# Optimization experiments

Measured on AMD Instinct MI355X. Metric: run time of the kernel, lower is better.

## Reference

```python
import jax, jax.numpy as jnp
import numpy as np

EPS_PROX = 5.0   # proximal epsilon from __init__
BN_EPS = 1e-5    # torch BatchNorm1d default eps
STRIDE = 3


def setup_inputs() -> dict:
    key = jax.random.key(0)
    ks = jax.random.split(key, 9)
    B, T, D = 64, 768, 128     # batch, timesteps, input_size
    E, H, O, K = 64, 128, 10, 3  # embedding_dim, hidden, output, kernel
    Tc = (T - K) // STRIDE + 1   # 256 conv output steps
    s_ih = 1.0 / np.sqrt(H)
    return {
        "inputs": jax.random.normal(ks[0], (B, T, D), jnp.float32),
        "r": jax.random.normal(ks[1], (B, E, Tc), jnp.float32),
        "conv_w": jax.random.normal(ks[2], (E, D, K), jnp.float32) * (1.0 / np.sqrt(D * K)),
        "conv_b": jnp.zeros((E,), jnp.float32),
        "bn_gamma": jnp.ones((E,), jnp.float32),
        "bn_beta": jnp.zeros((E,), jnp.float32),
        "w_ih": jax.random.normal(ks[3], (4 * H, E), jnp.float32) * s_ih,
        "w_hh": jax.random.normal(ks[4], (4 * H, H), jnp.float32) * s_ih,
        "b_ih": jax.random.normal(ks[5], (4 * H,), jnp.float32) * s_ih,
        "b_hh": jax.random.normal(ks[6], (4 * H,), jnp.float32) * s_ih,
        "lin_w": jax.random.normal(ks[7], (O, H), jnp.float32) * s_ih,
        "lin_b": jnp.zeros((O,), jnp.float32),
        "batch_size": B,
    }


def _forward(inputs, conv_w, conv_b, bn_gamma, bn_beta,
             w_ih, w_hh, b_ih, b_hh, lin_w, lin_b):
    # F.normalize(inputs, dim=2): L2 normalize feature dim
    nrm = jnp.sqrt(jnp.sum(inputs * inputs, axis=2, keepdims=True))
    x = inputs / jnp.maximum(nrm, 1e-12)
    x = jnp.transpose(x, (0, 2, 1))  # [B, D, T]
    # Conv1d(D -> E, kernel=3, stride=3)
    emb = jax.lax.conv_general_dilated(
        x, conv_w, window_strides=(STRIDE,), padding='VALID',
        dimension_numbers=('NCH', 'OIH', 'NCH')) + conv_b[None, :, None]
    # BatchNorm1d in training mode: batch stats over (B, T')
    mean = jnp.mean(emb, axis=(0, 2), keepdims=True)
    var = jnp.var(emb, axis=(0, 2), keepdims=True)
    emb = (emb - mean) * jax.lax.rsqrt(var + BN_EPS)
    emb = emb * bn_gamma[None, :, None] + bn_beta[None, :, None]
    act = jax.nn.relu(emb)               # [B, E, T']
    xs = jnp.transpose(act, (2, 0, 1))   # [T', B, E] scan over time

    H = w_hh.shape[1]
    Wi, Wf, Wg, Wo = jnp.split(w_ih, 4, axis=0)  # torch gate order i,f,g,o
    I_H = jnp.eye(H, dtype=inputs.dtype)

    def step(carry, x_t):
        h, c = carry
        z = x_t @ w_ih.T + b_ih + h @ w_hh.T + b_hh  # [B, 4H]
        zi, zf, zg, zo = jnp.split(z, 4, axis=1)
        i = jax.nn.sigmoid(zi)
        f = jax.nn.sigmoid(zf)
        g = jnp.tanh(zg)
        o = jax.nn.sigmoid(zo)
        s = f * c + i * g                            # pre-prox cell state
        # Analytic Jacobian G = ds/dx_t : [B, H, E]
        G = ((i * (1 - i) * g)[:, :, None] * Wi[None]
             + (f * (1 - f) * c)[:, :, None] * Wf[None]
             + (i * (1 - g * g))[:, :, None] * Wg[None])
        # Proximal update: c = (I + eps * G G^T)^{-1} s
        A = I_H + EPS_PROX * jnp.einsum('bhe,bke->bhk', G, G)
        c_new = jnp.linalg.solve(A, s[:, :, None])[:, :, 0]
        h_new = o * jnp.tanh(c_new)
        return (h_new, c_new), None

    B = xs.shape[1]
    init = (jnp.zeros((B, H), inputs.dtype), jnp.zeros((B, H), inputs.dtype))
    (h_last, _), _ = jax.lax.scan(step, init, xs)
    return h_last @ lin_w.T + lin_b  # [B, output_size]


def reference(inputs, r, conv_w, conv_b, bn_gamma, bn_beta,
              w_ih, w_hh, b_ih, b_hh, lin_w, lin_b, batch_size):
    # mode='ProxLSTM'; r and batch_size are unused in this branch (r is only
    # added to the embedding in 'plain' mode).
    return _forward(inputs, conv_w, conv_b, bn_gamma, bn_beta,
                    w_ih, w_hh, b_ih, b_hh, lin_w, lin_b)
```

## Files before the change

### kernel.cpp

```cpp
#include <hip/hip_runtime.h>
#include <math.h>

#define EPSP 5.0f
#define BNEPS 1e-5f
constexpr int B_  = 64;
constexpr int T_  = 768;
constexpr int D_  = 128;
constexpr int E_  = 64;
constexpr int H_  = 128;
constexpr int FH_ = 512;
constexpr int TC_ = 256;
constexpr int O_  = 10;

constexpr size_t EMB_OFF   = 0;
constexpr size_t SUM_OFF   = EMB_OFF + (size_t)B_ * TC_ * E_;
constexpr size_t SCL_OFF   = SUM_OFF + 128;
constexpr size_t CWT_OFF   = SCL_OFF + 128;
constexpr size_t WHIF_OFF  = CWT_OFF + (size_t)E_ * D_ * 3;
constexpr size_t WLO8F_OFF = WHIF_OFF + 32768;
constexpr size_t WTHI_OFF  = WLO8F_OFF + 16384;
constexpr size_t WTLO8_OFF = WTHI_OFF + 12288;
constexpr size_t ZX_OFF    = WTLO8_OFF + 6144;
constexpr size_t WS_FLOATS = ZX_OFF + (size_t)B_ * TC_ * FH_;

typedef __bf16 bf16x8 __attribute__((ext_vector_type(8)));
typedef float  floatx4 __attribute__((ext_vector_type(4)));

__device__ inline float fast_rcp(float x) { return __builtin_amdgcn_rcpf(x); }
__device__ inline float frsq(float x) { return __builtin_amdgcn_rsqf(x); }
__device__ inline float fexp2(float x) { return __builtin_amdgcn_exp2f(x); }
__device__ inline float rl(float v, int lane) {
  return __int_as_float(__builtin_amdgcn_readlane(__float_as_int(v), lane));
}
#define LOG2E 1.4426950408889634f
__device__ inline float fsigmoid(float x) { return fast_rcp(1.f + fexp2(-LOG2E * x)); }
__device__ inline float ftanh(float x) { return 1.f - 2.f * fast_rcp(1.f + fexp2(2.f * LOG2E * x)); }

__device__ inline unsigned char enc8(float v) {
  unsigned b = __float_as_uint(v);
  unsigned s = b >> 31;
  int e = (int)((b >> 23) & 0xFF) - 127;
  if (e < -6) return 0;
  unsigned m3 = (b >> 20) & 7;
  return (unsigned char)((s << 7) | ((unsigned)(e + 7) << 3) | m3);
}
#define S18 3.814697265625e-06f

__global__ void prep_kernel(const float* __restrict__ conv_w,
                            const float* __restrict__ w_hh,
                            float* __restrict__ ws) {
  int gid = blockIdx.x * blockDim.x + threadIdx.x;
  int nthr = gridDim.x * blockDim.x;
  for (int i = gid; i < 128; i += nthr) ws[SUM_OFF + i] = 0.f;
  __bf16* whiF = (__bf16*)(ws + WHIF_OFF);
  unsigned char* wlo8F = (unsigned char*)(ws + WLO8F_OFF);
  for (int s = gid; s < 512 * 128; s += nthr) {
    int st = s >> 7, r2 = s & 127, f = r2 >> 3, j = r2 & 7;
    int wv = st >> 6, lane = st & 63, m = lane & 15, q = lane >> 4;
    int rti = f >> 2, kt = f & 3;
    int R = wv * 64 + rti * 16 + m;
    int k = kt * 32 + q * 8 + j;
    float w = w_hh[(size_t)R * 128 + k];
    __bf16 hi = (__bf16)w;
    whiF[s] = hi;
    wlo8F[s] = enc8((w - (float)hi) * 16384.f);
  }
  for (int s = gid; s < E_ * D_ * 3; s += nthr) {
    int e = s / 384; int r = s - e * 384; int d = r / 3; int k = r - d * 3;
    ws[CWT_OFF + ((size_t)k * D_ + d) * E_ + e] = conv_w[s];
  }
}

__global__ __launch_bounds__(256) void conv_bn_kernel(const float* __restrict__ inputs,
                                                      const float* __restrict__ conv_b,
                                                      float* __restrict__ ws) {
  __shared__ float xin[48 * 129];
  __shared__ float rnorm[48];
  __shared__ float cwc[3 * 16 * 64];
  __shared__ float bnr1[256], bnr2[256];
  int tid = threadIdx.x;
  int bb = blockIdx.x >> 4, tcg = blockIdx.x & 15;
  const float* inp = inputs + ((size_t)bb * T_ + (size_t)tcg * 48) * D_;
  for (int idx = tid; idx < 48 * 128; idx += 256) {
    int r = idx >> 7, d = idx & 127;
    xin[r * 129 + d] = inp[idx];
  }
  __syncthreads();
  if (tid < 48) {
    float ss = 0.f;
    for (int d = 0; d < 128; ++d) { float v = xin[tid * 129 + d]; ss += v * v; }
    rnorm[tid] = 1.0f / fmaxf(sqrtf(ss), 1e-12f);
  }
  __syncthreads();
  for (int idx = tid; idx < 48 * 128; idx += 256) {
    int r = idx >> 7, d = idx & 127;
    xin[r * 129 + d] *= rnorm[r];
  }
  int e = tid & 63, tg = tid >> 6;
  float cb = conv_b[e];
  float acc[4];
#pragma unroll
  for (int q = 0; q < 4; ++q) acc[q] = cb;
  for (int ch = 0; ch < 8; ++ch) {
    __syncthreads();
    for (int idx = tid; idx < 3072; idx += 256) {
      int k = idx >> 10; int i2 = idx & 1023; int dd = i2 >> 6; int e2 = i2 & 63;
      cwc[idx] = ws[CWT_OFF + ((size_t)k * D_ + ch * 16 + dd) * E_ + e2];
    }
    __syncthreads();
    for (int dd = 0; dd < 16; ++dd) {
      int dcol = ch * 16 + dd;
#pragma unroll
      for (int k = 0; k < 3; ++k) {
        float w = cwc[(k * 16 + dd) * 64 + e];
#pragma unroll
        for (int q = 0; q < 4; ++q) {
          int tcl = tg * 4 + q;
          acc[q] += w * xin[(3 * tcl + k) * 129 + dcol];
        }
      }
    }
  }
  float ps = 0.f, pss = 0.f;
#pragma unroll
  for (int q = 0; q < 4; ++q) {
    int tcl = tg * 4 + q;
    ws[EMB_OFF + ((size_t)bb * TC_ + tcg * 16 + tcl) * E_ + e] = acc[q];
    ps += acc[q]; pss += acc[q] * acc[q];
  }
  bnr1[tg * 64 + e] = ps;
  bnr2[tg * 64 + e] = pss;
  __syncthreads();
  if (tid < 64) {
    float s1 = bnr1[tid] + bnr1[64 + tid] + bnr1[128 + tid] + bnr1[192 + tid];
    float s2 = bnr2[tid] + bnr2[64 + tid] + bnr2[128 + tid] + bnr2[192 + tid];
    atomicAdd(&ws[SUM_OFF + tid], s1);
    atomicAdd(&ws[SUM_OFF + 64 + tid], s2);
  }
}

__global__ void bn_finalize_kernel(const float* __restrict__ gamma,
                                   const float* __restrict__ beta,
                                   float* __restrict__ ws) {
  int e = threadIdx.x;
  if (e < 64) {
    const float n = (float)(B_ * TC_);
    float mean = ws[SUM_OFF + e] / n;
    float var = ws[SUM_OFF + 64 + e] / n - mean * mean;
    float sc = gamma[e] * rsqrtf(var + BNEPS);
    ws[SCL_OFF + e] = sc;
    ws[SCL_OFF + 64 + e] = beta[e] - mean * sc;
  }
}

__global__ __launch_bounds__(256) void zx_kernel(const float* __restrict__ w_ih,
                                                 const float* __restrict__ b_ih,
                                                 const float* __restrict__ b_hh,
                                                 float* __restrict__ ws) {
  __shared__ __align__(16) float actT[16 * 64];
  int tid = threadIdx.x;
  int bb = blockIdx.x >> 4, tg2 = blockIdx.x & 15;
  for (int idx = tid; idx < 1024; idx += 256) {
    int tl = idx >> 6, e2 = idx & 63;
    float v = ws[EMB_OFF + ((size_t)bb * TC_ + tg2 * 16 + tl) * E_ + e2];
    actT[idx] = fmaxf(v * ws[SCL_OFF + e2] + ws[SCL_OFF + 64 + e2], 0.f);
  }
  __syncthreads();
  int j0 = tid, j1 = tid + 256;
  float acc0[16], acc1[16];
  float bias0 = b_ih[j0] + b_hh[j0];
  float bias1 = b_ih[j1] + b_hh[j1];
#pragma unroll
  for (int tl = 0; tl < 16; ++tl) { acc0[tl] = bias0; acc1[tl] = bias1; }
  for (int e4 = 0; e4 < 16; ++e4) {
    float4 w0 = *(const float4*)(w_ih + (size_t)j0 * 64 + e4 * 4);
    float4 w1 = *(const float4*)(w_ih + (size_t)j1 * 64 + e4 * 4);
#pragma unroll
    for (int tl = 0; tl < 16; ++tl) {
      float4 a4 = *(const float4*)(actT + tl * 64 + e4 * 4);
      acc0[tl] += w0.x * a4.x + w0.y * a4.y + w0.z * a4.z + w0.w * a4.w;
      acc1[tl] += w1.x * a4.x + w1.y * a4.y + w1.z * a4.z + w1.w * a4.w;
    }
  }
#pragma unroll
  for (int tl = 0; tl < 16; ++tl) {
    size_t base = ZX_OFF + ((size_t)bb * TC_ + tg2 * 16 + tl) * FH_;
    ws[base + j0] = acc0[tl];
    ws[base + j1] = acc1[tl];
  }
}

template <int NCT>
__device__ inline void gram_do(int rt, int ct0, int lane,
                               const __bf16* GtHi, const __bf16* GtLo,
                               float* M_s, float* y_s) {
  int m = lane & 15, q = lane >> 4;
  bf16x8 AH[4], AL[4];
#pragma unroll
  for (int kt = 0; kt < 4; ++kt) {
    AH[kt] = *(const bf16x8*)(GtHi + (rt * 16 + m) * 136 + kt * 32 + q * 8);
    AL[kt] = *(const bf16x8*)(GtLo + (rt * 16 + m) * 136 + kt * 32 + q * 8);
  }
  floatx4 C[NCT];
#pragma unroll
  for (int ci = 0; ci < NCT; ++ci) C[ci] = (floatx4){0.f, 0.f, 0.f, 0.f};
#pragma unroll
  for (int ci = 0; ci < NCT; ++ci) {
#pragma unroll
    for (int kt = 0; kt < 4; ++kt) {
      bf16x8 BH = *(const bf16x8*)(GtHi + ((ct0 + ci) * 16 + m) * 136 + kt * 32 + q * 8);
      bf16x8 BL = *(const bf16x8*)(GtLo + ((ct0 + ci) * 16 + m) * 136 + kt * 32 + q * 8);
      C[ci] = __builtin_amdgcn_mfma_f32_16x16x32_bf16(AH[kt], BH, C[ci], 0, 0, 0);
      C[ci] = __builtin_amdgcn_mfma_f32_16x16x32_bf16(AH[kt], BL, C[ci], 0, 0, 0);
      C[ci] = __builtin_amdgcn_mfma_f32_16x16x32_bf16(AL[kt], BH, C[ci], 0, 0, 0);
    }
  }
#pragma unroll
  for (int ci = 0; ci < NCT; ++ci) {
    int ct = ct0 + ci;
#pragma unroll
    for (int reg = 0; reg < 4; ++reg) {
      int grow = rt * 16 + q * 4 + reg;
      if (ct < 4) {
        int gcol = ct * 16 + m;
        M_s[grow * 65 + gcol] = EPSP * C[ci][reg] + ((grow == gcol) ? 1.f : 0.f);
      } else if (m == 0) {
        y_s[grow] = C[ci][reg];
      }
    }
  }
}

#define LD8(dst, base) { float4 _a = *(const float4*)(base); float4 _b = *(const float4*)((base) + 4); \
  dst[0]=_a.x; dst[1]=_a.y; dst[2]=_a.z; dst[3]=_a.w; dst[4]=_b.x; dst[5]=_b.y; dst[6]=_b.z; dst[7]=_b.w; }

union U4L { uint4 u; long l[2]; };

__global__ __launch_bounds__(512, 2)
void scan_kernel(const float* __restrict__ w_ih,
                 const float* __restrict__ lin_w,
                 const float* __restrict__ lin_b,
                 const float* __restrict__ ws,
                 float* __restrict__ out) {
  __shared__ __align__(16) __bf16 GtHi[80 * 136], GtLo[80 * 136];
  __shared__ __align__(16) __bf16 hbH[128], hbL[128];
  __shared__ __align__(8)  unsigned char hb8[128];
  __shared__ float M_s[64 * 65];
  __shared__ float Lp2_s[2 * 16 * 64];
  __shared__ __align__(16) float z0_s[512], zx_s[512];
  __shared__ __align__(16) float s_s[128], o_s[128], c_s[128], h_s[128];
  __shared__ float y_s[64];
  __shared__ __align__(8) float x_s[64];
  __shared__ __align__(16) unsigned char W8L[512 * 128];

  const int tid = threadIdx.x;
  const int bb = blockIdx.x;
  const int lane = tid & 63;
  const int wv = tid >> 6;
  const int m = lane & 15, q = lane >> 4;
  const int hg = tid >> 5;
  const int ep = tid & 31;
  const int h0 = hg * 8, e0 = ep * 2;

  float Wr[3][2][8];
#pragma unroll
  for (int g = 0; g < 3; ++g)
#pragma unroll
    for (int e = 0; e < 2; ++e) {
      const float* bse = w_ih + ((size_t)(g * 128 + h0)) * 64 + e0 + e;
#pragma unroll
      for (int r = 0; r < 8; ++r) Wr[g][e][r] = bse[(size_t)r * 64];
    }

  bf16x8 WH[4][4];
  {
    const uint4* whip = (const uint4*)(ws + WHIF_OFF) + (size_t)tid * 16;
#pragma unroll
    for (int rti = 0; rti < 4; ++rti)
#pragma unroll
      for (int kt = 0; kt < 4; ++kt) {
        uint4 t4 = whip[rti * 4 + kt];
        WH[rti][kt] = __builtin_bit_cast(bf16x8, t4);
      }
  }
  {
    const uint4* src = (const uint4*)(ws + WLO8F_OFF) + (size_t)tid * 8;
    uint4* dst = (uint4*)W8L;
#pragma unroll
    for (int f = 0; f < 8; ++f) dst[f * 512 + tid] = src[f];
  }
  for (int i = tid; i < 15 * 136; i += 512) { GtHi[65 * 136 + i] = (__bf16)0.f; GtLo[65 * 136 + i] = (__bf16)0.f; }
  if (tid < 128) {
    c_s[tid] = 0.f; h_s[tid] = 0.f;
    hbH[tid] = (__bf16)0.f; hbL[tid] = (__bf16)0.f; hb8[tid] = 0;
  }
  const float* zxp = ws + ZX_OFF + (size_t)bb * TC_ * FH_;
  float dinv = 1.f;
  bf16x8 ZB;
#pragma unroll
  for (int j = 0; j < 8; ++j) ZB[j] = (__bf16)0.f;
  float zxcur = zxp[tid];
  __syncthreads();

  for (int t = 0; t < TC_; ++t) {
    {
      zx_s[tid] = zxcur;
      if (t + 1 < TC_) zxcur = zxp[(size_t)(t + 1) * FH_ + tid];
      long B8[4];
#pragma unroll
      for (int kt = 0; kt < 4; ++kt)
        B8[kt] = (m == 0) ? *(const long*)(hb8 + kt * 32 + q * 8) : 0L;
      floatx4 C[4];
#pragma unroll
      for (int h2 = 0; h2 < 2; ++h2) {
        U4L wa[4];
#pragma unroll
        for (int i = 0; i < 4; ++i) wa[i].u = ((const uint4*)W8L)[(h2 * 4 + i) * 512 + tid];
        floatx4 C8a = {0,0,0,0}, C8b = {0,0,0,0};
#pragma unroll
        for (int kt = 0; kt < 4; ++kt) {
          long A0 = wa[(0 * 4 + kt) >> 1].l[kt & 1];
          long A1 = wa[(1 * 4 + kt) >> 1].l[kt & 1];
          C8a = __builtin_amdgcn_mfma_f32_16x16x32_fp8_fp8(A0, B8[kt], C8a, 0, 0, 0);
          C8b = __builtin_amdgcn_mfma_f32_16x16x32_fp8_fp8(A1, B8[kt], C8b, 0, 0, 0);
        }
        C[h2 * 2 + 0] = C8a * S18;
        C[h2 * 2 + 1] = C8b * S18;
      }
#pragma unroll
      for (int p = 0; p < 2; ++p) {
        const __bf16* hb = p ? hbL : hbH;
#pragma unroll
        for (int kt = 0; kt < 4; ++kt) {
          bf16x8 Bf = (m == 0) ? *(const bf16x8*)(hb + kt * 32 + q * 8) : ZB;
#pragma unroll
          for (int rti = 0; rti < 4; ++rti)
            C[rti] = __builtin_amdgcn_mfma_f32_16x16x32_bf16(WH[rti][kt], Bf, C[rti], 0, 0, 0);
        }
      }
      if (m == 0) {
#pragma unroll
        for (int rti = 0; rti < 4; ++rti)
          *(floatx4*)(z0_s + wv * 64 + rti * 16 + q * 4) = C[rti];
      }
    }
    __syncthreads();
    float gva[2][8];
    {
      float zA[8], xA[8], zi[8], zf[8], zg[8], zo[8], cc[8];
      LD8(zA, z0_s + h0) LD8(xA, zx_s + h0)
#pragma unroll
      for (int r = 0; r < 8; ++r) zi[r] = zA[r] + xA[r];
      LD8(zA, z0_s + 128 + h0) LD8(xA, zx_s + 128 + h0)
#pragma unroll
      for (int r = 0; r < 8; ++r) zf[r] = zA[r] + xA[r];
      LD8(zA, z0_s + 256 + h0) LD8(xA, zx_s + 256 + h0)
#pragma unroll
      for (int r = 0; r < 8; ++r) zg[r] = zA[r] + xA[r];
      LD8(zA, z0_s + 384 + h0) LD8(xA, zx_s + 384 + h0)
#pragma unroll
      for (int r = 0; r < 8; ++r) zo[r] = zA[r] + xA[r];
      LD8(cc, c_s + h0)
      float a1[8], a2[8], a3[8], sv[8], ov[8];
#pragma unroll
      for (int r = 0; r < 8; ++r) {
        float ig = fsigmoid(zi[r]);
        float fg = fsigmoid(zf[r]);
        float gg = ftanh(zg[r]);
        sv[r] = fg * cc[r] + ig * gg;
        ov[r] = fsigmoid(zo[r]);
        a1[r] = ig * (1.f - ig) * gg;
        a2[r] = fg * (1.f - fg) * cc[r];
        a3[r] = ig * (1.f - gg * gg);
      }
      if (ep == 0) {
        *(float4*)(s_s + h0)     = (float4){sv[0], sv[1], sv[2], sv[3]};
        *(float4*)(s_s + h0 + 4) = (float4){sv[4], sv[5], sv[6], sv[7]};
        *(float4*)(o_s + h0)     = (float4){ov[0], ov[1], ov[2], ov[3]};
        *(float4*)(o_s + h0 + 4) = (float4){ov[4], ov[5], ov[6], ov[7]};
        bf16x8 sh, sl;
#pragma unroll
        for (int r = 0; r < 8; ++r) {
          __bf16 hi = (__bf16)sv[r];
          sh[r] = hi; sl[r] = (__bf16)(sv[r] - (float)hi);
        }
        *(bf16x8*)(GtHi + 64 * 136 + h0) = sh;
        *(bf16x8*)(GtLo + 64 * 136 + h0) = sl;
      }
#pragma unroll
      for (int e = 0; e < 2; ++e) {
        int col = e0 + e;
        bf16x8 gh, gl;
#pragma unroll
        for (int r = 0; r < 8; ++r) {
          float gv = a1[r] * Wr[0][e][r] + a2[r] * Wr[1][e][r] + a3[r] * Wr[2][e][r];
          gva[e][r] = gv;
          __bf16 hi = (__bf16)gv;
          gh[r] = hi; gl[r] = (__bf16)(gv - (float)hi);
        }
        *(bf16x8*)(GtHi + col * 136 + h0) = gh;
        *(bf16x8*)(GtLo + col * 136 + h0) = gl;
      }
    }
    __syncthreads();
    if (wv < 4) gram_do<3>(wv, 0, lane, GtHi, GtLo, M_s, y_s);
    else        gram_do<2>(wv - 4, 3, lane, GtHi, GtLo, M_s, y_s);
    __syncthreads();
#pragma unroll 1
    for (int pan = 0; pan < 4; ++pan) {
      int j0 = pan * 16;
      float* Lpw = Lp2_s + (pan & 1) * (16 * 64);
      float* Lpr = Lp2_s + (((pan & 1) ^ 1)) * (16 * 64);
      if (tid < 64) {
        float p[16];
#pragma unroll
        for (int jj = 0; jj < 16; ++jj) p[jj] = M_s[lane * 65 + j0 + jj];
#pragma unroll
        for (int jj = 0; jj < 16; ++jj) {
          float d  = rl(p[jj], j0 + jj);
          float rs = frsq(d);
          p[jj] *= rs;
          dinv = (lane == j0 + jj) ? rs : dinv;
          M_s[lane * 65 + j0 + jj] = (lane > j0 + jj) ? p[jj] * rs : 0.f;
          Lpw[jj * 64 + lane] = p[jj];
#pragma unroll
          for (int kk = jj + 1; kk < 16; ++kk) {
            float l = rl(p[jj], j0 + kk);
            p[kk] -= p[jj] * l;
          }
        }
        if (pan == 3) {
          float r = y_s[lane];
#pragma unroll 16
          for (int i = 0; i < 64; ++i) {
            float Ai = M_s[lane * 65 + i];
            r -= Ai * rl(r, i);
          }
          float tau = r * dinv * dinv;
#pragma unroll 16
          for (int i = 63; i >= 0; --i) {
            float Bi = M_s[i * 65 + lane];
            tau -= Bi * rl(tau, i);
          }
          x_s[lane] = tau;
        }
      } else if (pan >= 1) {
        int k0 = 16 * pan + 16;
        if (k0 < 64) {
          float Lrow[16];
#pragma unroll
          for (int jj = 0; jj < 16; ++jj) Lrow[jj] = Lpr[jj * 64 + lane];
          for (int k = k0 + (wv - 1); k < 64; k += 7) {
            float acc = M_s[lane * 65 + k];
#pragma unroll
            for (int jj = 0; jj < 16; ++jj) acc -= Lrow[jj] * Lpr[jj * 64 + k];
            M_s[lane * 65 + k] = acc;
          }
        }
      }
      __syncthreads();
      if (pan < 3) {
        float Lrow[16];
#pragma unroll
        for (int jj = 0; jj < 16; ++jj) Lrow[jj] = Lpw[jj * 64 + lane];
#pragma unroll
        for (int kk2 = 0; kk2 < 2; ++kk2) {
          int k = j0 + 16 + wv * 2 + kk2;
          float acc = M_s[lane * 65 + k];
#pragma unroll
          for (int jj = 0; jj < 16; ++jj) acc -= Lrow[jj] * Lpw[jj * 64 + k];
          M_s[lane * 65 + k] = acc;
        }
        __syncthreads();
      }
    }
    {
      float2 xl = *(const float2*)(x_s + e0);
      float u0[8];
#pragma unroll
      for (int r = 0; r < 8; ++r) u0[r] = gva[0][r] * xl.x + gva[1][r] * xl.y;
#pragma unroll
      for (int sft = 1; sft < 32; sft <<= 1)
#pragma unroll
        for (int r = 0; r < 8; ++r) u0[r] += __shfl_xor(u0[r], sft, 32);
      if (ep == 0) {
        float cn[8], hn[8];
        bf16x8 hh8, hl8;
        unsigned long long h8v = 0ULL;
#pragma unroll
        for (int r = 0; r < 8; ++r) {
          cn[r] = s_s[h0 + r] - EPSP * u0[r];
          hn[r] = o_s[h0 + r] * ftanh(cn[r]);
          __bf16 hi = (__bf16)hn[r];
          hh8[r] = hi; hl8[r] = (__bf16)(hn[r] - (float)hi);
          h8v |= ((unsigned long long)enc8(hn[r] * 16.f)) << (8 * r);
        }
        *(float4*)(c_s + h0)     = (float4){cn[0], cn[1], cn[2], cn[3]};
        *(float4*)(c_s + h0 + 4) = (float4){cn[4], cn[5], cn[6], cn[7]};
        *(float4*)(h_s + h0)     = (float4){hn[0], hn[1], hn[2], hn[3]};
        *(float4*)(h_s + h0 + 4) = (float4){hn[4], hn[5], hn[6], hn[7]};
        *(bf16x8*)(hbH + h0) = hh8;
        *(bf16x8*)(hbL + h0) = hl8;
        *(unsigned long long*)(hb8 + h0) = h8v;
      }
    }
    __syncthreads();
  }
  if (tid < O_) {
    float acc = lin_b[tid];
    for (int hh2 = 0; hh2 < 128; ++hh2) acc += h_s[hh2] * lin_w[tid * 128 + hh2];
    out[(size_t)bb * O_ + tid] = acc;
  }
}

extern "C" void kernel_launch(void* const* d_in, const int* in_sizes, int n_in,
                              void* d_out, int out_size, void* d_ws, size_t ws_size,
                              hipStream_t stream) {
  (void)in_sizes; (void)n_in; (void)out_size;
  const float* inputs  = (const float*)d_in[0];
  const float* conv_w  = (const float*)d_in[2];
  const float* conv_b  = (const float*)d_in[3];
  const float* gamma   = (const float*)d_in[4];
  const float* beta    = (const float*)d_in[5];
  const float* w_ih    = (const float*)d_in[6];
  const float* w_hh    = (const float*)d_in[7];
  const float* b_ih    = (const float*)d_in[8];
  const float* b_hh    = (const float*)d_in[9];
  const float* lin_w   = (const float*)d_in[10];
  const float* lin_b   = (const float*)d_in[11];
  float* out = (float*)d_out;
  float* ws  = (float*)d_ws;

  if (ws_size < WS_FLOATS * sizeof(float)) return;

  hipLaunchKernelGGL(prep_kernel, dim3(192), dim3(256), 0, stream, conv_w, w_hh, ws);
  hipLaunchKernelGGL(conv_bn_kernel, dim3(1024), dim3(256), 0, stream, inputs, conv_b, ws);
  hipLaunchKernelGGL(bn_finalize_kernel, dim3(1), dim3(64), 0, stream, gamma, beta, ws);
  hipLaunchKernelGGL(zx_kernel, dim3(1024), dim3(256), 0, stream, w_ih, b_ih, b_hh, ws);
  hipLaunchKernelGGL(scan_kernel, dim3(64), dim3(512), 0, stream, w_ih, lin_w, lin_b, ws, out);
}
```

Baseline: 4.632 ms.

## Switch Cholesky to LDL^T form and fuse BN finalize into zx kernel

The in-loop Cholesky factorization of the per-step 64x64 Gram system is rewritten as an LDL^T-style factorization that uses a reciprocal of the pivot instead of a reciprocal square root. Pivot reciprocals are stored in a small shared buffer and folded into the trailing-update rows. This shortens the serial dependency chain on the single factorizing wave. Separately, the BatchNorm finalize kernel is removed and its per-channel scale and shift are recomputed in each zx block, which saves one kernel launch at the cost of some redundant work per block.

New measurement: 4.897 ms. 1.06x slower.

```diff
diff --git a/kernel.cpp b/kernel.cpp
--- a/kernel.cpp
+++ b/kernel.cpp
@@ -139,31 +139,29 @@
   }
 }
 
-__global__ void bn_finalize_kernel(const float* __restrict__ gamma,
-                                   const float* __restrict__ beta,
-                                   float* __restrict__ ws) {
-  int e = threadIdx.x;
-  if (e < 64) {
-    const float n = (float)(B_ * TC_);
-    float mean = ws[SUM_OFF + e] / n;
-    float var = ws[SUM_OFF + 64 + e] / n - mean * mean;
-    float sc = gamma[e] * rsqrtf(var + BNEPS);
-    ws[SCL_OFF + e] = sc;
-    ws[SCL_OFF + 64 + e] = beta[e] - mean * sc;
-  }
-}
-
 __global__ __launch_bounds__(256) void zx_kernel(const float* __restrict__ w_ih,
                                                  const float* __restrict__ b_ih,
                                                  const float* __restrict__ b_hh,
+                                                 const float* __restrict__ gamma,
+                                                 const float* __restrict__ beta,
                                                  float* __restrict__ ws) {
   __shared__ __align__(16) float actT[16 * 64];
+  __shared__ float scl[128];
   int tid = threadIdx.x;
   int bb = blockIdx.x >> 4, tg2 = blockIdx.x & 15;
+  if (tid < 64) {
+    const float n = (float)(B_ * TC_);
+    float mean = ws[SUM_OFF + tid] / n;
+    float var = ws[SUM_OFF + 64 + tid] / n - mean * mean;
+    float sc = gamma[tid] * rsqrtf(var + BNEPS);
+    scl[tid] = sc;
+    scl[64 + tid] = beta[tid] - mean * sc;
+  }
+  __syncthreads();
   for (int idx = tid; idx < 1024; idx += 256) {
     int tl = idx >> 6, e2 = idx & 63;
     float v = ws[EMB_OFF + ((size_t)bb * TC_ + tg2 * 16 + tl) * E_ + e2];
-    actT[idx] = fmaxf(v * ws[SCL_OFF + e2] + ws[SCL_OFF + 64 + e2], 0.f);
+    actT[idx] = fmaxf(v * scl[e2] + scl[64 + e2], 0.f);
   }
   __syncthreads();
   int j0 = tid, j1 = tid + 256;
@@ -247,6 +245,7 @@
   __shared__ __align__(8)  unsigned char hb8[128];
   __shared__ float M_s[64 * 65];
   __shared__ float Lp2_s[2 * 16 * 64];
+  __shared__ float dp2_s[2 * 16];
   __shared__ __align__(16) float z0_s[512], zx_s[512];
   __shared__ __align__(16) float s_s[128], o_s[128], c_s[128], h_s[128];
   __shared__ float y_s[64];
@@ -411,6 +410,8 @@
       int j0 = pan * 16;
       float* Lpw = Lp2_s + (pan & 1) * (16 * 64);
       float* Lpr = Lp2_s + (((pan & 1) ^ 1)) * (16 * 64);
+      float* dpw = dp2_s + (pan & 1) * 16;
+      float* dpr = dp2_s + (((pan & 1) ^ 1)) * 16;
       if (tid < 64) {
         float p[16];
 #pragma unroll
@@ -418,15 +419,15 @@
 #pragma unroll
         for (int jj = 0; jj < 16; ++jj) {
           float d  = rl(p[jj], j0 + jj);
-          float rs = frsq(d);
-          p[jj] *= rs;
-          dinv = (lane == j0 + jj) ? rs : dinv;
-          M_s[lane * 65 + j0 + jj] = (lane > j0 + jj) ? p[jj] * rs : 0.f;
+          float di = fast_rcp(d);
+          dinv = (lane == j0 + jj) ? di : dinv;
+          M_s[lane * 65 + j0 + jj] = (lane > j0 + jj) ? p[jj] * di : 0.f;
           Lpw[jj * 64 + lane] = p[jj];
+          if (lane == j0 + jj) dpw[jj] = di;
 #pragma unroll
           for (int kk = jj + 1; kk < 16; ++kk) {
-            float l = rl(p[jj], j0 + kk);
-            p[kk] -= p[jj] * l;
+            float s = rl(p[jj], j0 + kk) * di;
+            p[kk] -= p[jj] * s;
           }
         }
         if (pan == 3) {
@@ -436,7 +437,7 @@
             float Ai = M_s[lane * 65 + i];
             r -= Ai * rl(r, i);
           }
-          float tau = r * dinv * dinv;
+          float tau = r * dinv;
 #pragma unroll 16
           for (int i = 63; i >= 0; --i) {
             float Bi = M_s[i * 65 + lane];
@@ -449,7 +450,7 @@
         if (k0 < 64) {
           float Lrow[16];
 #pragma unroll
-          for (int jj = 0; jj < 16; ++jj) Lrow[jj] = Lpr[jj * 64 + lane];
+          for (int jj = 0; jj < 16; ++jj) Lrow[jj] = Lpr[jj * 64 + lane] * dpr[jj];
           for (int k = k0 + (wv - 1); k < 64; k += 7) {
             float acc = M_s[lane * 65 + k];
 #pragma unroll
@@ -462,7 +463,7 @@
       if (pan < 3) {
         float Lrow[16];
 #pragma unroll
-        for (int jj = 0; jj < 16; ++jj) Lrow[jj] = Lpw[jj * 64 + lane];
+        for (int jj = 0; jj < 16; ++jj) Lrow[jj] = Lpw[jj * 64 + lane] * dpw[jj];
 #pragma unroll
         for (int kk2 = 0; kk2 < 2; ++kk2) {
           int k = j0 + 16 + wv * 2 + kk2;
@@ -535,7 +536,6 @@
 
   hipLaunchKernelGGL(prep_kernel, dim3(192), dim3(256), 0, stream, conv_w, w_hh, ws);
   hipLaunchKernelGGL(conv_bn_kernel, dim3(1024), dim3(256), 0, stream, inputs, conv_b, ws);
-  hipLaunchKernelGGL(bn_finalize_kernel, dim3(1), dim3(64), 0, stream, gamma, beta, ws);
-  hipLaunchKernelGGL(zx_kernel, dim3(1024), dim3(256), 0, stream, w_ih, b_ih, b_hh, ws);
+  hipLaunchKernelGGL(zx_kernel, dim3(1024), dim3(256), 0, stream, w_ih, b_ih, b_hh, gamma, beta, ws);
   hipLaunchKernelGGL(scan_kernel, dim3(64), dim3(512), 0, stream, w_ih, lin_w, lin_b, ws, out);
 }
```
